# Kernel tuning notes

Hardware: AMD Instinct MI355X
Metric: run time of the kernel (lower is better)

## Reference

```python
import jax, jax.numpy as jnp
import numpy as np
import math

# dims
BSZ, L, D = 2, 4096, 1024
EXPAND, DS, NH, NG, DC, CS = 2, 128, 32, 1, 4, 64
DI = EXPAND * D            # 2048
HP = DI // NH              # 64 headdim
D_IN_PROJ = 2 * DI + 2 * NG * DS + NH  # 4384
CONV_DIM = DI + 2 * NG * DS            # 2304
EPS = 1e-5


def setup_inputs() -> dict:
    key = jax.random.key(0)
    ks = jax.random.split(key, 10)
    u = jax.random.normal(ks[0], (BSZ, L, D), dtype=jnp.float32)
    W_in = jax.random.normal(ks[1], (D, D_IN_PROJ), dtype=jnp.float32) / math.sqrt(D)
    conv_w = jax.random.normal(ks[2], (CONV_DIM, DC), dtype=jnp.float32) / math.sqrt(DC)
    conv_b = jnp.zeros((CONV_DIM,), dtype=jnp.float32)
    # dt init as in module: dt ~ logspace(1e-3, 0.1), dt_bias = inv softplus
    dt = jnp.exp(jax.random.uniform(ks[3], (NH,)) * (math.log(0.1) - math.log(0.001)) + math.log(0.001))
    dt = jnp.clip(dt, 1e-4, None)
    dt_bias = dt + jnp.log(-jnp.expm1(-dt))
    A_log = jnp.log(jax.random.uniform(ks[4], (NH,), minval=1.0, maxval=16.0))
    norm_w = jnp.ones((DI,), dtype=jnp.float32)
    norm_b = jnp.zeros((DI,), dtype=jnp.float32)
    W_out = jax.random.normal(ks[5], (DI, D), dtype=jnp.float32) / math.sqrt(DI)
    return {"u": u, "W_in": W_in, "conv_w": conv_w, "conv_b": conv_b,
            "dt_bias": dt_bias, "A_log": A_log, "norm_w": norm_w,
            "norm_b": norm_b, "W_out": W_out}


def _segsum(x):
    # x: (..., l) -> (..., l, l), out[i,j] = sum_{j<t<=i} x[t], -inf above diag
    cs = jnp.cumsum(x, axis=-1)
    d = cs[..., :, None] - cs[..., None, :]
    n = x.shape[-1]
    mask = jnp.tril(jnp.ones((n, n), dtype=bool))
    return jnp.where(mask, d, -jnp.inf)


def _ssd(x, A, Bm, Cm):
    # x: (b,l,h,p) already scaled by dt; A: (b,l,h) = a*dt; Bm,Cm: (b,l,h,n)
    b, l, h, p = x.shape
    nc = l // CS
    x = x.reshape(b, nc, CS, h, p)
    A = A.reshape(b, nc, CS, h).transpose(0, 3, 1, 2)          # (b,h,c,s)
    Bm = Bm.reshape(b, nc, CS, h, -1)
    Cm = Cm.reshape(b, nc, CS, h, -1)
    A_cum = jnp.cumsum(A, axis=-1)                              # (b,h,c,s)
    Lmat = jnp.exp(_segsum(A))                                  # (b,h,c,s,s)
    # intra-chunk (diagonal block) output
    Yd = jnp.einsum('bclhn,bcshn,bhcls,bcshp->bclhp', Cm, Bm, Lmat, x)
    # per-chunk final states
    decay_states = jnp.exp(A_cum[..., -1:] - A_cum)             # (b,h,c,s)
    states = jnp.einsum('bcshn,bhcs,bcshp->bchpn', Bm, decay_states, x)
    # inter-chunk recurrence (parallel via segsum over chunk decays)
    A_chunk = jnp.pad(A_cum[..., -1], ((0, 0), (0, 0), (1, 0)))  # (b,h,c+1)
    decay_chunk = jnp.exp(_segsum(A_chunk))                      # (b,h,c+1,c+1)
    states0 = jnp.concatenate([jnp.zeros_like(states[:, :1]), states], axis=1)
    new_states = jnp.einsum('bhzc,bchpn->bzhpn', decay_chunk, states0)
    states_in = new_states[:, :-1]                               # (b,c,h,p,n)
    state_decay = jnp.exp(A_cum)                                 # (b,h,c,s)
    Yoff = jnp.einsum('bcshn,bchpn,bhcs->bcshp', Cm, states_in, state_decay)
    return (Yd + Yoff).reshape(b, l, h, p)


def _causal_dwconv(x, w, b):
    # x: (B,L,C), depthwise causal conv, kernel w: (C,K), bias b: (C,)
    k = w.shape[1]
    xp = jnp.pad(x, ((0, 0), (k - 1, 0), (0, 0)))
    seqlen = x.shape[1]
    out = b
    for i in range(k):  # small fixed kernel loop (K=4)
        out = out + xp[:, i:i + seqlen, :] * w[:, i]
    return out


def reference(u, W_in, conv_w, conv_b, dt_bias, A_log, norm_w, norm_b, W_out):
    b, l, _ = u.shape
    zxbcdt = u @ W_in                                  # (b,l,2*DI+2*NG*DS+NH)
    z = zxbcdt[..., :DI]
    xBC = zxbcdt[..., DI:DI + CONV_DIM]
    dt = jax.nn.softplus(zxbcdt[..., -NH:] + dt_bias)  # (b,l,h)
    A = -jnp.exp(A_log)                                # (h,)
    xBC = jax.nn.silu(_causal_dwconv(xBC, conv_w, conv_b))
    x = xBC[..., :DI].reshape(b, l, NH, HP)
    Bv = xBC[..., DI:DI + NG * DS].reshape(b, l, NG, DS)
    Cv = xBC[..., DI + NG * DS:].reshape(b, l, NG, DS)
    # broadcast groups to heads
    rep = NH // NG
    Bh = jnp.repeat(Bv, rep, axis=2)                   # (b,l,h,n)
    Ch = jnp.repeat(Cv, rep, axis=2)
    y = _ssd(x * dt[..., None], A * dt, Bh, Ch)        # (b,l,h,p)
    y = y.reshape(b, l, DI)
    y = y * jax.nn.silu(z)                             # gated
    mu = jnp.mean(y, axis=-1, keepdims=True)
    var = jnp.mean(jnp.square(y - mu), axis=-1, keepdims=True)
    y = (y - mu) * jax.lax.rsqrt(var + EPS) * norm_w + norm_b
    return y @ W_out
```

## Files before the change

kernel.cpp:

```cpp
#include <hip/hip_runtime.h>
#include <hip/hip_bf16.h>
#include <math.h>


namespace {

constexpr int kB   = 2;
constexpr int kL   = 4096;
constexpr int kDI  = 2048;
constexpr int kDS  = 128;
constexpr int kNH  = 32;
constexpr int kHP  = 64;
constexpr int kDC  = 4;
constexpr int kCS  = 64;
constexpr int kNC  = kL / kCS;
constexpr int kDProj   = 2 * kDI + 2 * kDS + kNH;
constexpr int kDProjP  = 4480;
constexpr int kConvDim = kDI + 2 * kDS;
constexpr int kRows = kB * kL;
constexpr float kEps = 1e-5f;
constexpr int kTS = 136;
constexpr int kWS = 72;

typedef __bf16 bf16x8 __attribute__((ext_vector_type(8)));
typedef float f32x4 __attribute__((ext_vector_type(4)));
typedef unsigned short ushort8 __attribute__((ext_vector_type(8)));

__device__ inline float bu2f(unsigned short u) {
  union { unsigned int i; float f; } x; x.i = ((unsigned int)u) << 16; return x.f;
}
__device__ inline unsigned short f2bu(float f) {
  __hip_bfloat16 h = __float2bfloat16(f);
  return *reinterpret_cast<unsigned short*>(&h);
}

__device__ inline void store_out(float* C, size_t i, float v) { C[i] = v; }
__device__ inline void store_out(unsigned short* C, size_t i, float v) { C[i] = f2bu(v); }

__device__ inline void gld_lds16(const unsigned short* g, unsigned short* l) {
  __builtin_amdgcn_global_load_lds(
      (const __attribute__((address_space(1))) unsigned int*)g,
      (__attribute__((address_space(3))) unsigned int*)l, 16, 0, 0);
}

__global__ void cast_kernel(const float4* __restrict__ in, ushort4* __restrict__ out, int n4) {
  int i = blockIdx.x * 256 + threadIdx.x;
  if (i >= n4) return;
  float4 v = in[i];
  ushort4 o;
  o.x = f2bu(v.x); o.y = f2bu(v.y); o.z = f2bu(v.z); o.w = f2bu(v.w);
  out[i] = o;
}

__global__ void transpose_cast(const float* __restrict__ in, unsigned short* __restrict__ out,
                               int R, int C, const float* __restrict__ scale) {
  __shared__ float t[32][33];
  const int c0 = blockIdx.x * 32;
  const int r0 = blockIdx.y * 32;
  const int tx = threadIdx.x & 31, ty = threadIdx.x >> 5;
  for (int rr = ty; rr < 32; rr += 8) {
    int c = c0 + tx;
    float v = (c < C) ? in[(size_t)(r0 + rr) * C + c] : 0.f;
    if (scale) v *= scale[r0 + rr];
    t[rr][tx] = v;
  }
  __syncthreads();
  for (int cc = ty; cc < 32; cc += 8) {
    int orow = c0 + cc;
    out[(size_t)orow * R + r0 + tx] = f2bu(t[tx][cc]);
  }
}

__global__ void colsum_kernel(const float* __restrict__ W2, const float* __restrict__ wv,
                              const float* __restrict__ bv,
                              float* __restrict__ t1, float* __restrict__ t2) {
  __shared__ float p1[4][64], p2[4][64];
  const int nl = threadIdx.x & 63;
  const int ks = threadIdx.x >> 6;
  const int n = blockIdx.x * 64 + nl;
  float s1 = 0.f, s2 = 0.f;
  for (int k = ks * 512; k < ks * 512 + 512; k++) {
    float v = W2[(size_t)k * 1024 + n];
    s1 += wv[k] * v;
    s2 += bv[k] * v;
  }
  p1[ks][nl] = s1; p2[ks][nl] = s2;
  __syncthreads();
  if (threadIdx.x < 64) {
    t1[blockIdx.x * 64 + threadIdx.x] =
        p1[0][threadIdx.x] + p1[1][threadIdx.x] + p1[2][threadIdx.x] + p1[3][threadIdx.x];
    t2[blockIdx.x * 64 + threadIdx.x] =
        p2[0][threadIdx.x] + p2[1][threadIdx.x] + p2[2][threadIdx.x] + p2[3][threadIdx.x];
  }
}

template <typename OutT, bool FOLD>
__global__ __launch_bounds__(256) void gemm_bt(const unsigned short* __restrict__ A,
                                               const unsigned short* __restrict__ Bt,
                                               OutT* __restrict__ C, int M, int N, int K,
                                               const float* __restrict__ mu,
                                               const float* __restrict__ rstd,
                                               const float* __restrict__ t1,
                                               const float* __restrict__ t2) {
  __shared__ __align__(16) unsigned short As[128 * 32];
  __shared__ __align__(16) unsigned short Bs[128 * 32];
  const int tid = threadIdx.x;
  const int wave = tid >> 6, lane = tid & 63;
  const int m0 = blockIdx.y * 128, n0 = blockIdx.x * 128;
  const int wr = (wave >> 1) * 64, wc = (wave & 1) * 64;
  const int st_row = lane >> 2;
  const int st_col = (((lane & 3) ^ ((st_row >> 1) & 3))) * 8;
  const unsigned short* pA[2];
  const unsigned short* pB[2];
  unsigned short* lA[2];
  unsigned short* lB[2];
#pragma unroll
  for (int r = 0; r < 2; r++) {
    int q = wave * 2 + r;
    pA[r] = A + (size_t)(m0 + q * 16 + st_row) * K + st_col;
    pB[r] = Bt + (size_t)(n0 + q * 16 + st_row) * K + st_col;
    lA[r] = &As[q * 512];
    lB[r] = &Bs[q * 512];
  }
  const int frag_row = lane & 15;
  const int rk = (((lane >> 4) ^ ((frag_row >> 1) & 3))) * 8;
  f32x4 acc[4][4] = {};
  for (int k0 = 0; k0 < K; k0 += 32) {
#pragma unroll
    for (int r = 0; r < 2; r++) {
      gld_lds16(pA[r] + k0, lA[r]);
      gld_lds16(pB[r] + k0, lB[r]);
    }
    asm volatile("s_waitcnt vmcnt(0)" ::: "memory");
    __syncthreads();
    bf16x8 af[4], bfr[4];
#pragma unroll
    for (int i = 0; i < 4; i++)
      af[i] = *(const bf16x8*)&As[(wr + i * 16 + frag_row) * 32 + rk];
#pragma unroll
    for (int j = 0; j < 4; j++)
      bfr[j] = *(const bf16x8*)&Bs[(wc + j * 16 + frag_row) * 32 + rk];
#pragma unroll
    for (int i = 0; i < 4; i++)
#pragma unroll
      for (int j = 0; j < 4; j++)
        acc[i][j] = __builtin_amdgcn_mfma_f32_16x16x32_bf16(af[i], bfr[j], acc[i][j], 0, 0, 0);
    __syncthreads();
  }
  const int crow = (lane >> 4) * 4;
  const int ccol = lane & 15;
#pragma unroll
  for (int i = 0; i < 4; i++) {
#pragma unroll
    for (int j = 0; j < 4; j++) {
      int n = n0 + wc + j * 16 + ccol;
      if (n < N) {
        float c1 = FOLD ? t1[n] : 0.f;
        float c2 = FOLD ? t2[n] : 0.f;
#pragma unroll
        for (int r = 0; r < 4; r++) {
          int m = m0 + wr + i * 16 + crow + r;
          float v = acc[i][j][r];
          if (FOLD) v = rstd[m] * (v - mu[m] * c1) + c2;
          store_out(C, (size_t)m * N + n, v);
        }
      }
    }
  }
}

__global__ void dt_kernel(const unsigned short* __restrict__ zxbcdt,
                          const float* __restrict__ dt_bias,
                          float* __restrict__ dtbuf) {
  int idx = blockIdx.x * 256 + threadIdx.x;
  if (idx >= kRows * kNH) return;
  int row = idx >> 5, h = idx & 31;
  float x = bu2f(zxbcdt[(size_t)row * kDProj + (kDProj - kNH) + h]) + dt_bias[h];
  dtbuf[idx] = (x > 15.f) ? x : log1pf(expf(x));
}

__global__ void conv_silu_kernel(const unsigned short* __restrict__ zxbcdt,
                                 const float* __restrict__ conv_w,
                                 const float* __restrict__ conv_b,
                                 unsigned short* __restrict__ xbc_act) {
  int c4 = blockIdx.x * 256 + threadIdx.x;
  if (c4 >= kConvDim / 4) return;
  const int c = c4 * 4;
  const int r0 = blockIdx.y * 8;
  const int l0 = r0 & (kL - 1);
  float4 w[4];
  float bias[4];
#pragma unroll
  for (int q = 0; q < 4; q++) {
    w[q] = ((const float4*)conv_w)[c + q];
    bias[q] = conv_b[c + q];
  }
  float v[11][4];
#pragma unroll
  for (int i = 0; i < 11; i++) {
    int l = l0 - 3 + i;
    if (l >= 0) {
      ushort4 t = *(const ushort4*)&zxbcdt[(size_t)(r0 - 3 + i) * kDProj + kDI + c];
      v[i][0] = bu2f(t.x); v[i][1] = bu2f(t.y); v[i][2] = bu2f(t.z); v[i][3] = bu2f(t.w);
    } else {
      v[i][0] = v[i][1] = v[i][2] = v[i][3] = 0.f;
    }
  }
#pragma unroll
  for (int j = 0; j < 8; j++) {
    ushort4 o;
    unsigned short* op = (unsigned short*)&o;
#pragma unroll
    for (int q = 0; q < 4; q++) {
      float a = bias[q] + v[j][q] * w[q].x + v[j + 1][q] * w[q].y +
                v[j + 2][q] * w[q].z + v[j + 3][q] * w[q].w;
      op[q] = f2bu(a / (1.f + expf(-a)));
    }
    *(ushort4*)&xbc_act[(size_t)(r0 + j) * kConvDim + c] = o;
  }
}

__global__ __launch_bounds__(256) void chunk_state_kernel(
    const unsigned short* __restrict__ xbc_act,
    const float* __restrict__ dtbuf,
    const float* __restrict__ A_log,
    unsigned short* __restrict__ states,
    float* __restrict__ asum) {
  const int id = blockIdx.x;
  const int h = id & 31;
  const int c = (id >> 5) & (kNC - 1);
  const int b = id >> 11;
  const int tid = threadIdx.x;
  const int wave = tid >> 6, lane = tid & 63;
  __shared__ __align__(16) unsigned short sBT[kDS * kWS];
  __shared__ __align__(16) unsigned short sxd[kCS * kWS];
  __shared__ float s_dt[kCS];
  __shared__ float s_acum[kCS];
  const int l0 = b * kL + c * kCS;
  if (tid < kCS) s_dt[tid] = dtbuf[(size_t)(l0 + tid) * kNH + h];
  __syncthreads();
  if (tid == 0) {
    float A = -expf(A_log[h]);
    float run = 0.f;
    for (int s = 0; s < kCS; s++) { run += A * s_dt[s]; s_acum[s] = run; }
    asum[id] = run;
  }
  __syncthreads();
  const float total = s_acum[kCS - 1];
  for (int e = tid; e < kCS * kDS; e += 256) {
    int s = e >> 7, n = e & 127;
    sBT[n * kWS + s] = xbc_act[(size_t)(l0 + s) * kConvDim + kDI + n];
  }
  for (int e = tid; e < kCS * kHP; e += 256) {
    int s = e >> 6, p = e & 63;
    float xv = bu2f(xbc_act[(size_t)(l0 + s) * kConvDim + h * kHP + p]);
    sxd[p * kWS + s] = f2bu(xv * s_dt[s] * expf(total - s_acum[s]));
  }
  __syncthreads();
  const int arow = wave * 16 + (lane & 15);
  const int fk = (lane >> 4) * 8;
  f32x4 acc[8] = {};
#pragma unroll
  for (int kk = 0; kk < 2; kk++) {
    bf16x8 a = *(const bf16x8*)&sxd[arow * kWS + kk * 32 + fk];
#pragma unroll
    for (int j = 0; j < 8; j++) {
      bf16x8 bb = *(const bf16x8*)&sBT[(j * 16 + (lane & 15)) * kWS + kk * 32 + fk];
      acc[j] = __builtin_amdgcn_mfma_f32_16x16x32_bf16(a, bb, acc[j], 0, 0, 0);
    }
  }
  const int prow = wave * 16 + (lane >> 4) * 4;
  const int ncol = lane & 15;
  size_t base = (size_t)id * (kHP * kDS);
#pragma unroll
  for (int j = 0; j < 8; j++)
#pragma unroll
    for (int r = 0; r < 4; r++)
      states[base + (size_t)(prow + r) * kDS + j * 16 + ncol] = f2bu(acc[j][r]);
}

__global__ void scan_kernel(unsigned short* __restrict__ states,
                            const float* __restrict__ asum) {
  const int blk = blockIdx.x;
  const int seg = blk & 7;
  const int bh = blk >> 3;
  const int h = bh & 31, b = bh >> 5;
  const int e4 = seg * 256 + threadIdx.x;
  const size_t cstride = (size_t)kNH * 2048;
  ushort4* p = (ushort4*)states + ((size_t)(b * kNC) * kNH + h) * 2048 + e4;
  const float* ap = asum + (b * kNC) * kNH + h;
  float c0 = 0.f, c1 = 0.f, c2 = 0.f, c3 = 0.f;
  ushort4 t = p[0];
  float dec = expf(ap[0]);
  for (int c = 0; c < kNC; c++) {
    ushort4 tn = t;
    float decn = dec;
    if (c + 1 < kNC) {
      tn = p[(size_t)(c + 1) * cstride];
      decn = expf(ap[(c + 1) * kNH]);
    }
    ushort4 o;
    o.x = f2bu(c0); o.y = f2bu(c1); o.z = f2bu(c2); o.w = f2bu(c3);
    p[(size_t)c * cstride] = o;
    c0 = c0 * dec + bu2f(t.x);
    c1 = c1 * dec + bu2f(t.y);
    c2 = c2 * dec + bu2f(t.z);
    c3 = c3 * dec + bu2f(t.w);
    t = tn; dec = decn;
  }
}

__global__ __launch_bounds__(256) void y_kernel(
    const unsigned short* __restrict__ xbc_act,
    const unsigned short* __restrict__ zxbcdt,
    const unsigned short* __restrict__ states_in,
    const float* __restrict__ dtbuf,
    const float* __restrict__ A_log,
    unsigned short* __restrict__ ybuf,
    float* __restrict__ pS, float* __restrict__ pQ) {
  const int id = blockIdx.x;
  const int hg = id & 7;
  const int c = (id >> 3) & (kNC - 1);
  const int b = id >> 9;
  const int tid = threadIdx.x;
  const int wave = tid >> 6, lane = tid & 63;
  __shared__ __align__(16) unsigned short sC[kCS * kTS];
  __shared__ __align__(16) unsigned short sB[kCS * kTS];
  __shared__ __align__(16) unsigned short sxd[kCS * kWS];
  __shared__ __align__(16) unsigned short sW[kCS * kWS];
  __shared__ float s_dt[4][kCS];
  __shared__ float s_acum[4][kCS];
  const int l0 = b * kL + c * kCS;
  {
    int hh = tid >> 6, s = tid & 63;
    s_dt[hh][s] = dtbuf[(size_t)(l0 + s) * kNH + hg * 4 + hh];
  }
  __syncthreads();
  if (tid < 4) {
    float A = -expf(A_log[hg * 4 + tid]);
    float run = 0.f;
    for (int s = 0; s < kCS; s++) { run += A * s_dt[tid][s]; s_acum[tid][s] = run; }
  }
  for (int e = tid; e < kCS * 16; e += 256) {
    int row = e >> 4, c8 = (e & 15) * 8;
    size_t rb = (size_t)(l0 + row) * kConvDim;
    *(ushort8*)&sB[row * kTS + c8] = *(const ushort8*)&xbc_act[rb + kDI + c8];
    *(ushort8*)&sC[row * kTS + c8] = *(const ushort8*)&xbc_act[rb + kDI + kDS + c8];
  }
  __syncthreads();
  const int arow = wave * 16 + (lane & 15);
  const int fk = (lane >> 4) * 8;
  f32x4 accG[4] = {};
#pragma unroll
  for (int kk = 0; kk < 4; kk++) {
    bf16x8 a = *(const bf16x8*)&sC[arow * kTS + kk * 32 + fk];
#pragma unroll
    for (int j = 0; j < 4; j++) {
      bf16x8 bb = *(const bf16x8*)&sB[(j * 16 + (lane & 15)) * kTS + kk * 32 + fk];
      accG[j] = __builtin_amdgcn_mfma_f32_16x16x32_bf16(a, bb, accG[j], 0, 0, 0);
    }
  }
  const int lrow = wave * 16 + (lane >> 4) * 4;
  const size_t sbase = (size_t)((b * kNC + c) * kNH) * (kHP * kDS);
  float rS[4] = {}, rQ[4] = {};
  for (int hh = 0; hh < 4; hh++) {
    const int h = hg * 4 + hh;
    __syncthreads();
    for (int e = tid; e < kCS * kHP; e += 256) {
      int s = e >> 6, p = e & 63;
      float xv = bu2f(xbc_act[(size_t)(l0 + s) * kConvDim + h * kHP + p]);
      sxd[p * kWS + s] = f2bu(xv * s_dt[hh][s]);
    }
#pragma unroll
    for (int j = 0; j < 4; j++) {
      int scol = j * 16 + (lane & 15);
      float as = s_acum[hh][scol];
#pragma unroll
      for (int r = 0; r < 4; r++) {
        int l = lrow + r;
        float w = (scol <= l) ? accG[j][r] * expf(s_acum[hh][l] - as) : 0.f;
        sW[l * kWS + scol] = f2bu(w);
      }
    }
    for (int e = tid; e < kCS * 16; e += 256) {
      int row = e >> 4, c8 = (e & 15) * 8;
      *(ushort8*)&sB[row * kTS + c8] =
          *(const ushort8*)&states_in[sbase + (size_t)h * (kHP * kDS) + row * kDS + c8];
    }
    __syncthreads();
    f32x4 accY[4] = {};
#pragma unroll
    for (int kk = 0; kk < 2; kk++) {
      bf16x8 a = *(const bf16x8*)&sW[arow * kWS + kk * 32 + fk];
#pragma unroll
      for (int j = 0; j < 4; j++) {
        bf16x8 bb = *(const bf16x8*)&sxd[(j * 16 + (lane & 15)) * kWS + kk * 32 + fk];
        accY[j] = __builtin_amdgcn_mfma_f32_16x16x32_bf16(a, bb, accY[j], 0, 0, 0);
      }
    }
    f32x4 accO[4] = {};
#pragma unroll
    for (int kk = 0; kk < 4; kk++) {
      bf16x8 a = *(const bf16x8*)&sC[arow * kTS + kk * 32 + fk];
#pragma unroll
      for (int j = 0; j < 4; j++) {
        bf16x8 bb = *(const bf16x8*)&sB[(j * 16 + (lane & 15)) * kTS + kk * 32 + fk];
        accO[j] = __builtin_amdgcn_mfma_f32_16x16x32_bf16(a, bb, accO[j], 0, 0, 0);
      }
    }
#pragma unroll
    for (int r = 0; r < 4; r++) {
      int l = lrow + r;
      float el = expf(s_acum[hh][l]);
      size_t zrow = (size_t)(l0 + l) * kDProj + h * kHP;
      size_t yrow = (size_t)(l0 + l) * kDI + h * kHP;
#pragma unroll
      for (int j = 0; j < 4; j++) {
        int p = j * 16 + (lane & 15);
        float yv = accY[j][r] + el * accO[j][r];
        float z = bu2f(zxbcdt[zrow + p]);
        yv *= z / (1.f + expf(-z));
        rS[r] += yv;
        rQ[r] += yv * yv;
        ybuf[yrow + p] = f2bu(yv);
      }
    }
  }
#pragma unroll
  for (int m = 1; m < 16; m <<= 1) {
#pragma unroll
    for (int r = 0; r < 4; r++) {
      rS[r] += __shfl_xor(rS[r], m);
      rQ[r] += __shfl_xor(rQ[r], m);
    }
  }
  if ((lane & 15) == 0) {
#pragma unroll
    for (int r = 0; r < 4; r++) {
      int row = l0 + lrow + r;
      pS[(size_t)row * 8 + hg] = rS[r];
      pQ[(size_t)row * 8 + hg] = rQ[r];
    }
  }
}

__global__ void ln_reduce(const float* __restrict__ pS, const float* __restrict__ pQ,
                          float* __restrict__ mu, float* __restrict__ rstd) {
  int row = blockIdx.x * 256 + threadIdx.x;
  if (row >= kRows) return;
  float s = 0.f, q = 0.f;
#pragma unroll
  for (int i = 0; i < 8; i++) { s += pS[(size_t)row * 8 + i]; q += pQ[(size_t)row * 8 + i]; }
  float m = s / kDI;
  mu[row] = m;
  rstd[row] = rsqrtf(q / kDI - m * m + kEps);
}

}

extern "C" void kernel_launch(void* const* d_in, const int* in_sizes, int n_in,
                              void* d_out, int out_size, void* d_ws, size_t ws_size,
                              hipStream_t stream) {
  const float* u       = (const float*)d_in[0];
  const float* W_in    = (const float*)d_in[1];
  const float* conv_w  = (const float*)d_in[2];
  const float* conv_b  = (const float*)d_in[3];
  const float* dt_bias = (const float*)d_in[4];
  const float* A_log   = (const float*)d_in[5];
  const float* norm_w  = (const float*)d_in[6];
  const float* norm_b  = (const float*)d_in[7];
  const float* W_out   = (const float*)d_in[8];
  float* out = (float*)d_out;

  char* ws = (char*)d_ws;
  size_t off = 0;
  auto alloc = [&](size_t bytes) {
    void* p = ws + off;
    off += (bytes + 255) & ~(size_t)255;
    return p;
  };
  unsigned short* zxbcdt = (unsigned short*)alloc((size_t)kRows * kDProj * 2);
  unsigned short* xbc    = (unsigned short*)alloc((size_t)kRows * kConvDim * 2);
  float* dtb             = (float*)alloc((size_t)kRows * kNH * 4);
  float* asum            = (float*)alloc((size_t)kB * kNC * kNH * 4);
  unsigned short* A1     = (unsigned short*)alloc((size_t)kRows * 1024 * 2);
  unsigned short* Bt1    = (unsigned short*)alloc((size_t)kDProjP * 1024 * 2);
  unsigned short* states = (unsigned short*)alloc((size_t)kB * kNC * kNH * kHP * kDS * 2);
  unsigned short* Bt2    = (unsigned short*)alloc((size_t)1024 * kDI * 2);
  unsigned short* ybuf   = (unsigned short*)alloc((size_t)kRows * kDI * 2);
  float* mu              = (float*)alloc((size_t)kRows * 4);
  float* rstd            = (float*)alloc((size_t)kRows * 4);
  float* t1              = (float*)alloc(1024 * 4);
  float* t2              = (float*)alloc(1024 * 4);
  float* pS              = (float*)alloc((size_t)kRows * 8 * 4);
  float* pQ              = (float*)alloc((size_t)kRows * 8 * 4);
  (void)ws_size; (void)in_sizes; (void)n_in; (void)out_size;

  cast_kernel<<<(kRows * 1024 / 4 + 255) / 256, 256, 0, stream>>>(
      (const float4*)u, (ushort4*)A1, kRows * 1024 / 4);
  transpose_cast<<<dim3(kDProjP / 32, 1024 / 32), 256, 0, stream>>>(
      W_in, Bt1, 1024, kDProj, nullptr);
  transpose_cast<<<dim3(1024 / 32, 2048 / 32), 256, 0, stream>>>(
      W_out, Bt2, 2048, 1024, norm_w);
  colsum_kernel<<<16, 256, 0, stream>>>(W_out, norm_w, norm_b, t1, t2);
  gemm_bt<unsigned short, false><<<dim3(kDProjP / 128, kRows / 128), 256, 0, stream>>>(
      A1, Bt1, zxbcdt, kRows, kDProj, 1024, nullptr, nullptr, nullptr, nullptr);
  dt_kernel<<<(kRows * kNH + 255) / 256, 256, 0, stream>>>(zxbcdt, dt_bias, dtb);
  conv_silu_kernel<<<dim3(3, kRows / 8), 256, 0, stream>>>(zxbcdt, conv_w, conv_b, xbc);
  chunk_state_kernel<<<kB * kNC * kNH, 256, 0, stream>>>(xbc, dtb, A_log, states, asum);
  scan_kernel<<<kB * kNH * 8, 256, 0, stream>>>(states, asum);
  y_kernel<<<kB * kNC * 8, 256, 0, stream>>>(xbc, zxbcdt, states, dtb, A_log, ybuf, pS, pQ);
  ln_reduce<<<kRows / 256, 256, 0, stream>>>(pS, pQ, mu, rstd);
  gemm_bt<float, true><<<dim3(1024 / 128, kRows / 128), 256, 0, stream>>>(
      ybuf, Bt2, out, kRows, 1024, 2048, mu, rstd, t1, t2);
}
```

Baseline: 466.8 us.

## Replace input projection GEMM with 256x256-tile 8-wave pipelined MFMA kernel

Adds a new bf16 GEMM for the input projection that uses 256x256 tiles, 512 threads and double-buffered LDS filled by direct global-to-LDS loads. The k-loop is split into four phases, each interleaving MFMA work with the next stage's loads, and uses raised wave priority and a swizzled workgroup order for L2 locality. Padding of the projection width is raised to a multiple of 256, which adds some wasted columns. The larger tiles cut global traffic per FLOP and aim to hide memory latency, at the cost of higher LDS and register use per workgroup.

```diff
diff --git a/kernel.cpp b/kernel.cpp
--- a/kernel.cpp
+++ b/kernel.cpp
@@ -15,7 +15,7 @@
 constexpr int kCS  = 64;
 constexpr int kNC  = kL / kCS;
 constexpr int kDProj   = 2 * kDI + 2 * kDS + kNH;
-constexpr int kDProjP  = 4480;
+constexpr int kDProjP  = 4608;
 constexpr int kConvDim = kDI + 2 * kDS;
 constexpr int kRows = kB * kL;
 constexpr float kEps = 1e-5f;
@@ -93,6 +93,124 @@
         p2[0][threadIdx.x] + p2[1][threadIdx.x] + p2[2][threadIdx.x] + p2[3][threadIdx.x];
   }
 }
+
+#define STG_A(bs, h, t)                                                         \
+  gld_lds16(srcA[h][0] + (t) * 64, &sA[bs][(h) * 8192 + wave * 1024]);          \
+  gld_lds16(srcA[h][1] + (t) * 64, &sA[bs][(h) * 8192 + wave * 1024 + 512]);
+#define STG_B(bs, h, t)                                                         \
+  gld_lds16(srcB[h][0] + (t) * 64, &sB[bs][(h) * 8192 + wave * 1024]);          \
+  gld_lds16(srcB[h][1] + (t) * 64, &sB[bs][(h) * 8192 + wave * 1024 + 512]);
+
+#define PHASE(q_, curA_, curB_, STAGE_STMT, TAIL_STMT)                          \
+  {                                                                             \
+    const int ha_ = (q_) >> 1, hb_ = (q_) & 1;                                  \
+    bf16x8 af_[4][2], bf_[2][2];                                                \
+    _Pragma("unroll")                                                           \
+    for (int i_ = 0; i_ < 4; i_++) {                                            \
+      af_[i_][0] = *(const bf16x8*)&(curA_)[ha_ * 8192 + rbaseA + i_ * 1024 + sk0]; \
+      af_[i_][1] = *(const bf16x8*)&(curA_)[ha_ * 8192 + rbaseA + i_ * 1024 + sk1]; \
+    }                                                                           \
+    _Pragma("unroll")                                                           \
+    for (int j_ = 0; j_ < 2; j_++) {                                            \
+      bf_[j_][0] = *(const bf16x8*)&(curB_)[hb_ * 8192 + rbaseB + j_ * 1024 + sk0]; \
+      bf_[j_][1] = *(const bf16x8*)&(curB_)[hb_ * 8192 + rbaseB + j_ * 1024 + sk1]; \
+    }                                                                           \
+    STAGE_STMT                                                                  \
+    __builtin_amdgcn_s_barrier();                                               \
+    asm volatile("s_waitcnt lgkmcnt(0)" ::: "memory");                          \
+    __builtin_amdgcn_sched_barrier(0);                                          \
+    __builtin_amdgcn_s_setprio(1);                                              \
+    _Pragma("unroll")                                                           \
+    for (int i_ = 0; i_ < 4; i_++)                                              \
+      _Pragma("unroll")                                                         \
+      for (int j_ = 0; j_ < 2; j_++) {                                          \
+        acc[ha_ * 4 + i_][hb_ * 2 + j_] = __builtin_amdgcn_mfma_f32_16x16x32_bf16( \
+            af_[i_][0], bf_[j_][0], acc[ha_ * 4 + i_][hb_ * 2 + j_], 0, 0, 0);  \
+        acc[ha_ * 4 + i_][hb_ * 2 + j_] = __builtin_amdgcn_mfma_f32_16x16x32_bf16( \
+            af_[i_][1], bf_[j_][1], acc[ha_ * 4 + i_][hb_ * 2 + j_], 0, 0, 0);  \
+      }                                                                         \
+    __builtin_amdgcn_s_setprio(0);                                              \
+    __builtin_amdgcn_sched_barrier(0);                                          \
+    TAIL_STMT                                                                   \
+    __builtin_amdgcn_s_barrier();                                               \
+  }
+
+__global__ __launch_bounds__(512, 2) void gemm_bt_8p(
+    const unsigned short* __restrict__ A, const unsigned short* __restrict__ Bt,
+    unsigned short* __restrict__ C, int Nreal) {
+  constexpr int K = 1024, NT = 16;
+  constexpr int GX = kDProjP / 256;
+  constexpr int NWG = GX * (kRows / 256);
+  __shared__ __align__(16) unsigned short sA[2][16384];
+  __shared__ __align__(16) unsigned short sB[2][16384];
+  const int tid = (int)threadIdx.x;
+  const int wave = tid >> 6, lane = tid & 63;
+  const int wm = wave >> 2, wn = wave & 3;
+  const int orig = (int)blockIdx.y * GX + (int)blockIdx.x;
+  const int swz = (orig & 7) * (NWG / 8) + (orig >> 3);
+  const int m0 = (swz / GX) * 256;
+  const int n0 = (swz % GX) * 256;
+  const int l8 = lane >> 3, s8 = lane & 7;
+  const unsigned short* srcA[2][2];
+  const unsigned short* srcB[2][2];
+#pragma unroll
+  for (int h = 0; h < 2; h++)
+#pragma unroll
+    for (int cc = 0; cc < 2; cc++) {
+      const int lrow = (wave * 2 + cc) * 8 + l8;
+      const int slot = s8 ^ (lrow & 7);
+      const int rA = (lrow & 63) + h * 64 + ((lrow >> 6) << 7);
+      const int rB = (lrow & 31) + h * 32 + ((lrow >> 5) << 6);
+      srcA[h][cc] = A + (size_t)(m0 + rA) * K + slot * 8;
+      srcB[h][cc] = Bt + (size_t)(n0 + rB) * K + slot * 8;
+    }
+  const int fr = lane & 15, c4 = lane >> 4;
+  const int sk0 = (c4 ^ (fr & 7)) * 8;
+  const int sk1 = ((4 | c4) ^ (fr & 7)) * 8;
+  const int rbaseA = (wm * 64 + fr) * 64;
+  const int rbaseB = (wn * 32 + fr) * 64;
+  f32x4 acc[8][4] = {};
+  unsigned short* const a0 = &sA[0][0];
+  unsigned short* const a1 = &sA[1][0];
+  unsigned short* const b0 = &sB[0][0];
+  unsigned short* const b1 = &sB[1][0];
+  STG_A(0, 0, 0) STG_B(0, 0, 0) STG_A(0, 1, 0) STG_B(0, 1, 0)
+  STG_A(1, 0, 1) STG_B(1, 0, 1)
+  asm volatile("s_waitcnt vmcnt(4)" ::: "memory");
+  __builtin_amdgcn_s_barrier();
+  for (int u = 0; u < NT; u += 2) {
+    const int t1 = u + 1, t2 = u + 2, t3 = u + 3;
+    PHASE(0, a0, b0, { STG_A(1, 1, t1) }, {})
+    PHASE(1, a0, b0, { STG_B(1, 1, t1) }, {})
+    PHASE(2, a0, b0, { if (t2 < NT) { STG_A(0, 0, t2) } }, {})
+    PHASE(3, a0, b0, { if (t2 < NT) { STG_B(0, 0, t2) } },
+          { if (t2 < NT) { asm volatile("s_waitcnt vmcnt(4)" ::: "memory"); }
+            else { asm volatile("s_waitcnt vmcnt(0)" ::: "memory"); } })
+    PHASE(0, a1, b1, { if (t2 < NT) { STG_A(0, 1, t2) } }, {})
+    PHASE(1, a1, b1, { if (t2 < NT) { STG_B(0, 1, t2) } }, {})
+    PHASE(2, a1, b1, { if (t3 < NT) { STG_A(1, 0, t3) } }, {})
+    PHASE(3, a1, b1, { if (t3 < NT) { STG_B(1, 0, t3) } },
+          { if (t3 < NT) { asm volatile("s_waitcnt vmcnt(4)" ::: "memory"); }
+            else { asm volatile("s_waitcnt vmcnt(0)" ::: "memory"); } })
+  }
+  const int crow = c4 * 4;
+#pragma unroll
+  for (int ii = 0; ii < 8; ii++) {
+    const int mbase = m0 + wm * 128 + (ii >> 2) * 64 + (ii & 3) * 16 + crow;
+#pragma unroll
+    for (int jj = 0; jj < 4; jj++) {
+      const int n = n0 + wn * 64 + (jj >> 1) * 32 + (jj & 1) * 16 + fr;
+      if (n < Nreal) {
+#pragma unroll
+        for (int r = 0; r < 4; r++)
+          C[(size_t)(mbase + r) * Nreal + n] = f2bu(acc[ii][jj][r]);
+      }
+    }
+  }
+}
+#undef PHASE
+#undef STG_A
+#undef STG_B
 
 template <typename OutT, bool FOLD>
 __global__ __launch_bounds__(256) void gemm_bt(const unsigned short* __restrict__ A,
@@ -503,8 +621,8 @@
   transpose_cast<<<dim3(1024 / 32, 2048 / 32), 256, 0, stream>>>(
       W_out, Bt2, 2048, 1024, norm_w);
   colsum_kernel<<<16, 256, 0, stream>>>(W_out, norm_w, norm_b, t1, t2);
-  gemm_bt<unsigned short, false><<<dim3(kDProjP / 128, kRows / 128), 256, 0, stream>>>(
-      A1, Bt1, zxbcdt, kRows, kDProj, 1024, nullptr, nullptr, nullptr, nullptr);
+  gemm_bt_8p<<<dim3(kDProjP / 256, kRows / 256), 512, 0, stream>>>(
+      A1, Bt1, zxbcdt, kDProj);
   dt_kernel<<<(kRows * kNH + 255) / 256, 256, 0, stream>>>(zxbcdt, dt_bias, dtb);
   conv_silu_kernel<<<dim3(3, kRows / 8), 256, 0, stream>>>(zxbcdt, conv_w, conv_b, xbc);
   chunk_state_kernel<<<kB * kNC * kNH, 256, 0, stream>>>(xbc, dtb, A_log, states, asum);
```

Result: no change. 472.1 us (+1.1%).

## Deepen GEMM K-tile to 64 with XOR LDS swizzle and grouped block order

Applied to the files above, without the earlier changes.

The bf16 MFMA GEMM now stages a 64-wide K slice per iteration instead of 32, which halves the number of barrier/wait cycles per tile, and uses a new 8-way XOR swizzle for the LDS layout. Workgroup IDs are remapped in a strided pattern to improve L2 reuse across neighbouring tiles, and launch bounds request three blocks per CU. LDS usage doubles and register pressure rises, which could limit occupancy. There is still no double buffering, so global loads and MFMA work remain serialized within each iteration.

```diff
diff --git a/kernel.cpp b/kernel.cpp
--- a/kernel.cpp
+++ b/kernel.cpp
@@ -95,56 +95,75 @@
 }
 
 template <typename OutT, bool FOLD>
-__global__ __launch_bounds__(256) void gemm_bt(const unsigned short* __restrict__ A,
-                                               const unsigned short* __restrict__ Bt,
-                                               OutT* __restrict__ C, int M, int N, int K,
-                                               const float* __restrict__ mu,
-                                               const float* __restrict__ rstd,
-                                               const float* __restrict__ t1,
-                                               const float* __restrict__ t2) {
-  __shared__ __align__(16) unsigned short As[128 * 32];
-  __shared__ __align__(16) unsigned short Bs[128 * 32];
+__global__ __launch_bounds__(256, 3) void gemm_bt(const unsigned short* __restrict__ A,
+                                                  const unsigned short* __restrict__ Bt,
+                                                  OutT* __restrict__ C, int M, int N, int K,
+                                                  const float* __restrict__ mu,
+                                                  const float* __restrict__ rstd,
+                                                  const float* __restrict__ t1,
+                                                  const float* __restrict__ t2) {
+  __shared__ __align__(16) unsigned short As[128 * 64];
+  __shared__ __align__(16) unsigned short Bs[128 * 64];
   const int tid = threadIdx.x;
   const int wave = tid >> 6, lane = tid & 63;
-  const int m0 = blockIdx.y * 128, n0 = blockIdx.x * 128;
+  const int nwg = (int)(gridDim.x * gridDim.y);
+  const int orig = (int)(blockIdx.y * gridDim.x + blockIdx.x);
+  const int swz = (orig & 7) * (nwg >> 3) + (orig >> 3);
+  const int bx = swz % (int)gridDim.x, by = swz / (int)gridDim.x;
+  const int m0 = by * 128, n0 = bx * 128;
   const int wr = (wave >> 1) * 64, wc = (wave & 1) * 64;
-  const int st_row = lane >> 2;
-  const int st_col = (((lane & 3) ^ ((st_row >> 1) & 3))) * 8;
-  const unsigned short* pA[2];
-  const unsigned short* pB[2];
-  unsigned short* lA[2];
-  unsigned short* lB[2];
-#pragma unroll
-  for (int r = 0; r < 2; r++) {
-    int q = wave * 2 + r;
-    pA[r] = A + (size_t)(m0 + q * 16 + st_row) * K + st_col;
-    pB[r] = Bt + (size_t)(n0 + q * 16 + st_row) * K + st_col;
+  const int l8 = lane >> 3, s8 = lane & 7;
+  const unsigned short* pA[4];
+  const unsigned short* pB[4];
+  unsigned short* lA[4];
+  unsigned short* lB[4];
+#pragma unroll
+  for (int r = 0; r < 4; r++) {
+    int q = wave * 4 + r;
+    pA[r] = A + (size_t)(m0 + q * 8 + l8) * K + (s8 ^ l8) * 8;
+    pB[r] = Bt + (size_t)(n0 + q * 8 + l8) * K + (s8 ^ l8) * 8;
     lA[r] = &As[q * 512];
     lB[r] = &Bs[q * 512];
   }
-  const int frag_row = lane & 15;
-  const int rk = (((lane >> 4) ^ ((frag_row >> 1) & 3))) * 8;
+  const int fr = lane & 15;
+  const int c4 = lane >> 4;
+  const int sk0 = (c4 ^ (fr & 7)) * 8;
+  const int sk1 = ((4 | c4) ^ (fr & 7)) * 8;
   f32x4 acc[4][4] = {};
-  for (int k0 = 0; k0 < K; k0 += 32) {
-#pragma unroll
-    for (int r = 0; r < 2; r++) {
+  for (int k0 = 0; k0 < K; k0 += 64) {
+#pragma unroll
+    for (int r = 0; r < 4; r++) {
       gld_lds16(pA[r] + k0, lA[r]);
       gld_lds16(pB[r] + k0, lB[r]);
     }
     asm volatile("s_waitcnt vmcnt(0)" ::: "memory");
     __syncthreads();
-    bf16x8 af[4], bfr[4];
-#pragma unroll
-    for (int i = 0; i < 4; i++)
-      af[i] = *(const bf16x8*)&As[(wr + i * 16 + frag_row) * 32 + rk];
-#pragma unroll
-    for (int j = 0; j < 4; j++)
-      bfr[j] = *(const bf16x8*)&Bs[(wc + j * 16 + frag_row) * 32 + rk];
-#pragma unroll
-    for (int i = 0; i < 4; i++)
-#pragma unroll
-      for (int j = 0; j < 4; j++)
-        acc[i][j] = __builtin_amdgcn_mfma_f32_16x16x32_bf16(af[i], bfr[j], acc[i][j], 0, 0, 0);
+    {
+      bf16x8 af0[4], bf0[4];
+#pragma unroll
+      for (int i = 0; i < 4; i++) {
+        af0[i] = *(const bf16x8*)&As[(wr + i * 16 + fr) * 64 + sk0];
+        bf0[i] = *(const bf16x8*)&Bs[(wc + i * 16 + fr) * 64 + sk0];
+      }
+#pragma unroll
+      for (int i = 0; i < 4; i++)
+#pragma unroll
+        for (int j = 0; j < 4; j++)
+          acc[i][j] = __builtin_amdgcn_mfma_f32_16x16x32_bf16(af0[i], bf0[j], acc[i][j], 0, 0, 0);
+    }
+    {
+      bf16x8 af1[4], bf1[4];
+#pragma unroll
+      for (int i = 0; i < 4; i++) {
+        af1[i] = *(const bf16x8*)&As[(wr + i * 16 + fr) * 64 + sk1];
+        bf1[i] = *(const bf16x8*)&Bs[(wc + i * 16 + fr) * 64 + sk1];
+      }
+#pragma unroll
+      for (int i = 0; i < 4; i++)
+#pragma unroll
+        for (int j = 0; j < 4; j++)
+          acc[i][j] = __builtin_amdgcn_mfma_f32_16x16x32_bf16(af1[i], bf1[j], acc[i][j], 0, 0, 0);
+    }
     __syncthreads();
   }
   const int crow = (lane >> 4) * 4;
```

Result: faster. 437.6 us (-6.2%).
